# Optimization experiments

Measured on AMD Instinct MI355X. Metric: run time of the kernel, lower is better.

Reference implementation:

```python
import jax, jax.numpy as jnp
import numpy as np

N_NODES = 50000
N_EDGES = 800000
D_FEAT = 64
D_HID = 64
N_CLASSES = 16


def gcn_conv(x, row, col, ew, W, b, n_nodes):
    """PyG GCNConv (normalize=True, add_self_loops=True) with edge weights.
    out[c] = sum_{(r,c) in E+selfloops} d^-1/2[r] * w * d^-1/2[c] * (x @ W)[r] + b
    """
    h = x @ W  # [N, out]
    loop = jnp.arange(n_nodes)
    row = jnp.concatenate([row, loop])
    col = jnp.concatenate([col, loop])
    w = jnp.concatenate([ew, jnp.ones((n_nodes,), dtype=ew.dtype)])
    deg = jax.ops.segment_sum(w, col, num_segments=n_nodes)  # in-degree (weighted)
    dinv = jnp.where(deg > 0, jax.lax.rsqrt(deg), 0.0)
    norm = dinv[row] * w * dinv[col]  # [E+N]
    msgs = norm[:, None] * h[row]  # [E+N, out]
    out = jax.ops.segment_sum(msgs, col, num_segments=n_nodes)
    return out + b


def setup_inputs() -> dict:
    key = jax.random.key(0)
    ks = jax.random.split(key, 12)
    x = jax.random.normal(ks[0], (N_NODES, D_FEAT), dtype=jnp.float32)
    edge_index = jax.random.randint(ks[1], (2, N_EDGES), 0, N_NODES, dtype=jnp.int64)
    edge_attr = jax.random.uniform(ks[2], (N_EDGES,), dtype=jnp.float32)
    s1 = 1.0 / np.sqrt(D_FEAT)
    s2 = 1.0 / np.sqrt(D_HID)
    W1 = jax.random.uniform(ks[3], (D_FEAT, D_HID), minval=-s1, maxval=s1, dtype=jnp.float32)
    b1 = jnp.zeros((D_HID,), dtype=jnp.float32)
    W2 = jax.random.uniform(ks[4], (D_HID, D_HID), minval=-s2, maxval=s2, dtype=jnp.float32)
    b2 = jnp.zeros((D_HID,), dtype=jnp.float32)
    Wm1 = jax.random.uniform(ks[5], (D_HID, D_HID), minval=-s2, maxval=s2, dtype=jnp.float32)
    bm1 = jax.random.uniform(ks[6], (D_HID,), minval=-s2, maxval=s2, dtype=jnp.float32)
    Wm2 = jax.random.uniform(ks[7], (D_HID, N_CLASSES), minval=-s2, maxval=s2, dtype=jnp.float32)
    bm2 = jax.random.uniform(ks[8], (N_CLASSES,), minval=-s2, maxval=s2, dtype=jnp.float32)
    return {"x": x, "edge_index": edge_index, "edge_attr": edge_attr,
            "W1": W1, "b1": b1, "W2": W2, "b2": b2,
            "Wm1": Wm1, "bm1": bm1, "Wm2": Wm2, "bm2": bm2}


def reference(x, edge_index, edge_attr, W1, b1, W2, b2, Wm1, bm1, Wm2, bm2):
    # eval-mode forward: dropout is identity
    n = x.shape[0]
    row, col = edge_index[0], edge_index[1]
    h = jax.nn.relu(gcn_conv(x, row, col, edge_attr, W1, b1, n))
    h = jax.nn.relu(gcn_conv(h, row, col, edge_attr, W2, b2, n))
    h = jax.nn.relu(h @ Wm1 + bm1)
    logits = h @ Wm2 + bm2
    return jax.nn.sigmoid(logits)
```

## Files before the change

kernel.cpp:

```cpp
#include <hip/hip_runtime.h>
#include <hip/hip_fp16.h>
#include <math.h>

#define D 64
#define CAP 48
#define PSZ 512
#define NBIN 98
#define BCAP 9216
#define TSTRIDE 16
#define FILLB 256
#define CHUNKMAX 3136


__global__ void __launch_bounds__(256, 2) k_mm1_fill(
        const float* __restrict__ X, const float* __restrict__ W1,
        __half* __restrict__ Y, int n, int mmBlocks,
        const int* __restrict__ row, const int* __restrict__ col,
        const float* __restrict__ ew, int* __restrict__ tails,
        unsigned long long* __restrict__ binsG, int E) {
    __shared__ unsigned long long buf[CHUNKMAX];
    __shared__ int hist[NBIN], startS[NBIN], curS[NBIN], baseS[NBIN];

    if (blockIdx.x < mmBlocks) {
        int lane = threadIdx.x & 63;
        float wreg[64];
#pragma unroll
        for (int k = 0; k < 64; ++k) wreg[k] = W1[k * 64 + lane];
        int wv  = blockIdx.x * 4 + (threadIdx.x >> 6);
        int nwv = mmBlocks * 4;
        const float4* x4 = (const float4*)X;
        for (int r = wv; r < n; r += nwv) {
            float acc = 0.f;
#pragma unroll
            for (int j = 0; j < 16; ++j) {
                float4 v = x4[r * 16 + j];
                acc += v.x * wreg[4 * j + 0] + v.y * wreg[4 * j + 1]
                     + v.z * wreg[4 * j + 2] + v.w * wreg[4 * j + 3];
            }
            Y[r * 64 + lane] = __float2half(acc);
        }
    } else {
        int fb  = blockIdx.x - mmBlocks;
        int tid = threadIdx.x;
        int chunk = (E + FILLB - 1) / FILLB;
        int e0 = fb * chunk;
        int e1 = min(e0 + chunk, E);
        int tot = e1 - e0;

        for (int i = tid; i < NBIN; i += 256) hist[i] = 0;
        __syncthreads();
        for (int e = e0 + tid; e < e1; e += 256)
            atomicAdd(&hist[col[e] >> 9], 1);
        __syncthreads();
        if (tid < NBIN) {
            int s = 0;
            for (int i = 0; i < tid; ++i) s += hist[i];
            startS[tid] = s;
            curS[tid]   = s;
            baseS[tid]  = atomicAdd(&tails[tid * TSTRIDE], hist[tid]);
        }
        __syncthreads();
        for (int e = e0 + tid; e < e1; e += 256) {
            int c = col[e];
            int b = c >> 9;
            int p = atomicAdd(&curS[b], 1);
            unsigned lo = ((unsigned)row[e] << 9) | (unsigned)(c & (PSZ - 1));
            buf[p] = ((unsigned long long)__float_as_uint(ew[e]) << 32) | lo;
        }
        __syncthreads();
        for (int i = tid; i < tot; i += 256) {
            int loB = 0, hiB = NBIN - 1;
            while (loB < hiB) {
                int mid = (loB + hiB + 1) >> 1;
                if (startS[mid] <= i) loB = mid; else hiB = mid - 1;
            }
            int dst = baseS[loB] + (i - startS[loB]);
            if (dst < BCAP)
                binsG[(size_t)loB * BCAP + dst] = buf[i];
        }
    }
}


__global__ void k_binscatter(const unsigned long long* __restrict__ binsG,
                             const int* __restrict__ tails,
                             int* __restrict__ cnt, int2* __restrict__ bucket, int n) {
    __shared__ int lc[PSZ];
    int bin = blockIdx.x, tid = threadIdx.x;
    for (int i = tid; i < PSZ; i += 256) lc[i] = 0;
    __syncthreads();
    int m = tails[bin * TSTRIDE];
    if (m > BCAP) m = BCAP;
    const unsigned long long* src = binsG + (size_t)bin * BCAP;
    int base = bin * PSZ;
    for (int i = tid; i < m; i += 256) {
        unsigned long long v = src[i];
        unsigned lo = (unsigned)v;
        int cOff = lo & (PSZ - 1);
        int r    = (int)(lo >> 9);
        int p = atomicAdd(&lc[cOff], 1);
        if (p < CAP)
            bucket[(size_t)(base + cOff) * CAP + p] = make_int2(r, (int)(v >> 32));
    }
    __syncthreads();
    for (int i = tid; i < PSZ; i += 256) {
        int node = base + i;
        if (node < n) cnt[node] = lc[i];
    }
}


__global__ void k_dinv_scale(const int* __restrict__ cnt, const int2* __restrict__ bucket,
                             __half* __restrict__ xw1, float* __restrict__ dinv, int n) {
    int lane = threadIdx.x & 63;
    int wv = blockIdx.x * 4 + (threadIdx.x >> 6);
    int nw = gridDim.x * 4;
    for (int node = wv; node < n; node += nw) {
        int c = cnt[node]; if (c > CAP) c = CAP;
        float s = 0.f;
        if (lane < c) s = __int_as_float(bucket[node * CAP + lane].y);
#pragma unroll
        for (int off = 32; off; off >>= 1) s += __shfl_xor(s, off, 64);
        float dv = rsqrtf(1.0f + s);
        if (lane == 0) dinv[node] = dv;
        int idx = node * 64 + lane;
        xw1[idx] = __float2half(dv * __half2float(xw1[idx]));
    }
}


__device__ __forceinline__ float gather_node(const __half* __restrict__ xw,
                                             const int* __restrict__ cnt,
                                             const int2* __restrict__ bucket,
                                             float d, float bb, int node, int lane) {
    float acc0 = __half2float(xw[node * 64 + lane]);
    float acc1 = 0.f, acc2 = 0.f, acc3 = 0.f;
    int p  = node * CAP;
    int c  = cnt[node]; if (c > CAP) c = CAP;
    int pe = p + c;
    for (; p + 8 <= pe; p += 8) {
        int2 e0 = bucket[p + 0];
        int2 e1 = bucket[p + 1];
        int2 e2 = bucket[p + 2];
        int2 e3 = bucket[p + 3];
        int2 e4 = bucket[p + 4];
        int2 e5 = bucket[p + 5];
        int2 e6 = bucket[p + 6];
        int2 e7 = bucket[p + 7];
        float v0 = __half2float(xw[e0.x * 64 + lane]);
        float v1 = __half2float(xw[e1.x * 64 + lane]);
        float v2 = __half2float(xw[e2.x * 64 + lane]);
        float v3 = __half2float(xw[e3.x * 64 + lane]);
        float v4 = __half2float(xw[e4.x * 64 + lane]);
        float v5 = __half2float(xw[e5.x * 64 + lane]);
        float v6 = __half2float(xw[e6.x * 64 + lane]);
        float v7 = __half2float(xw[e7.x * 64 + lane]);
        acc0 += __int_as_float(e0.y) * v0;
        acc1 += __int_as_float(e1.y) * v1;
        acc2 += __int_as_float(e2.y) * v2;
        acc3 += __int_as_float(e3.y) * v3;
        acc0 += __int_as_float(e4.y) * v4;
        acc1 += __int_as_float(e5.y) * v5;
        acc2 += __int_as_float(e6.y) * v6;
        acc3 += __int_as_float(e7.y) * v7;
    }
    for (; p + 4 <= pe; p += 4) {
        int2 e0 = bucket[p + 0];
        int2 e1 = bucket[p + 1];
        int2 e2 = bucket[p + 2];
        int2 e3 = bucket[p + 3];
        acc0 += __int_as_float(e0.y) * __half2float(xw[e0.x * 64 + lane]);
        acc1 += __int_as_float(e1.y) * __half2float(xw[e1.x * 64 + lane]);
        acc2 += __int_as_float(e2.y) * __half2float(xw[e2.x * 64 + lane]);
        acc3 += __int_as_float(e3.y) * __half2float(xw[e3.x * 64 + lane]);
    }
    for (; p < pe; ++p) {
        int2 e = bucket[p];
        acc0 += __int_as_float(e.y) * __half2float(xw[e.x * 64 + lane]);
    }
    return d * ((acc0 + acc1) + (acc2 + acc3)) + bb;
}


__global__ void k_gather_mm(const __half* __restrict__ xw, const float* __restrict__ dinv,
                            const float* __restrict__ b, const int* __restrict__ cnt,
                            const int2* __restrict__ bucket, const float* __restrict__ W,
                            __half* __restrict__ out, int n) {
    __shared__ float ws[64][64];
    __shared__ float hs[4][64];
    int tid = threadIdx.x;
    for (int i = tid; i < 4096; i += 256) ws[i >> 6][i & 63] = W[i];

    int lane = tid & 63, w = tid >> 6;
    float bb = b[lane];
    int ngrp = (n + 3) >> 2;
    for (int g = blockIdx.x; g < ngrp; g += gridDim.x) {
        int node = g * 4 + w;
        float d = (node < n) ? dinv[node] : 0.f;
        __syncthreads();
        if (node < n)
            hs[w][lane] = fmaxf(gather_node(xw, cnt, bucket, d, bb, node, lane), 0.0f);
        __syncthreads();
        if (node < n) {
            float s = 0.f;
#pragma unroll
            for (int k = 0; k < 64; ++k) s += hs[w][k] * ws[k][lane];
            out[node * 64 + lane] = __float2half(d * s);
        }
    }
}


__global__ void k_gather_head(const __half* __restrict__ xw, const float* __restrict__ dinv,
                              const float* __restrict__ b, const int* __restrict__ cnt,
                              const int2* __restrict__ bucket,
                              const float* __restrict__ Wm1, const float* __restrict__ bm1,
                              const float* __restrict__ Wm2, const float* __restrict__ bm2,
                              float* __restrict__ out, int n) {
    __shared__ __half w1h[64][64];
    __shared__ float w2[64][16];
    __shared__ float sb1[64];
    __shared__ float sb2[16];
    __shared__ float h2s[4][64];
    __shared__ float h3s[4][64];
    int tid = threadIdx.x;
    for (int i = tid; i < 4096; i += 256) w1h[i >> 6][i & 63] = __float2half(Wm1[i]);
    for (int i = tid; i < 1024; i += 256) w2[i >> 4][i & 15] = Wm2[i];
    if (tid < 64) sb1[tid] = bm1[tid];
    if (tid < 16) sb2[tid] = bm2[tid];

    int lane = tid & 63, w = tid >> 6;
    float bb = b[lane];
    int ngrp = (n + 3) >> 2;
    for (int g = blockIdx.x; g < ngrp; g += gridDim.x) {
        int node = g * 4 + w;
        float d = (node < n) ? dinv[node] : 0.f;
        __syncthreads();
        if (node < n)
            h2s[w][lane] = fmaxf(gather_node(xw, cnt, bucket, d, bb, node, lane), 0.0f);
        __syncthreads();
        if (node < n) {
            float s = sb1[lane];
#pragma unroll
            for (int k = 0; k < 64; ++k) s += h2s[w][k] * __half2float(w1h[k][lane]);
            h3s[w][lane] = fmaxf(s, 0.0f);
        }
        __syncthreads();
        if (node < n && lane < 16) {
            float s2 = sb2[lane];
#pragma unroll
            for (int k = 0; k < 64; ++k) s2 += h3s[w][k] * w2[k][lane];
            out[node * 16 + lane] = 1.0f / (1.0f + expf(-s2));
        }
    }
}


extern "C" void kernel_launch(void* const* d_in, const int* in_sizes, int n_in,
                              void* d_out, int out_size, void* d_ws, size_t ws_size,
                              hipStream_t stream) {
    const float* x   = (const float*)d_in[0];
    const int*   ei  = (const int*)d_in[1];
    const float* ew  = (const float*)d_in[2];
    const float* W1  = (const float*)d_in[3];
    const float* b1  = (const float*)d_in[4];
    const float* W2  = (const float*)d_in[5];
    const float* b2  = (const float*)d_in[6];
    const float* Wm1 = (const float*)d_in[7];
    const float* bm1 = (const float*)d_in[8];
    const float* Wm2 = (const float*)d_in[9];
    const float* bm2 = (const float*)d_in[10];

    int n = in_sizes[0] / D;
    int E = in_sizes[1] / 2;
    const int* row = ei;
    const int* col = ei + E;

    char* wsb = (char*)d_ws;
    int2*   bucket = (int2*)wsb;
    __half* xw1    = (__half*)(bucket + (size_t)n * CAP);
    unsigned long long* binsG = (unsigned long long*)(xw1 + (size_t)n * D);
    __half* xw2    = (__half*)binsG;
    int*    cnt    = (int*)(binsG + (size_t)NBIN * BCAP);
    float*  dinv   = (float*)(cnt + n);
    int*    tails  = (int*)(dinv + n);
    float*  outp   = (float*)d_out;

    int mmBlocks = 1024;

    hipMemsetAsync(tails, 0, (size_t)NBIN * TSTRIDE * sizeof(int), stream);
    k_mm1_fill<<<mmBlocks + FILLB, 256, 0, stream>>>(x, W1, xw1, n, mmBlocks,
                                                     row, col, ew, tails, binsG, E);
    k_binscatter<<<NBIN, 256, 0, stream>>>(binsG, tails, cnt, bucket, n);
    k_dinv_scale<<<2048, 256, 0, stream>>>(cnt, bucket, xw1, dinv, n);
    k_gather_mm<<<2048, 256, 0, stream>>>(xw1, dinv, b1, cnt, bucket, W2, xw2, n);
    k_gather_head<<<2048, 256, 0, stream>>>(xw2, dinv, b2, cnt, bucket,
                                            Wm1, bm1, Wm2, bm2, outp, n);
}
```

Baseline: 250.6 us.

## Finer binning, fuse degree sum into binscatter, wave-level barriers in gathers

Halves the bin size so twice as many bins and fill blocks are used, and caches edge data in registers so the fill pass reads each edge once. It also uses a two-level prefix sum. The weighted degree sum and rsqrt move into binscatter using shared-memory float atomics, and the scale step becomes a vectorized elementwise kernel. The gather kernels swap block-wide __syncthreads for wave barriers and load bucket entries with nontemporal loads. Float atomic summation order changes rounding slightly, and the CHUNKMAX clamp silently drops edges if E grows beyond the sized capacity.

```diff
diff --git a/kernel.cpp b/kernel.cpp
--- a/kernel.cpp
+++ b/kernel.cpp
@@ -4,12 +4,15 @@
 
 #define D 64
 #define CAP 48
-#define PSZ 512
-#define NBIN 98
-#define BCAP 9216
+#define PSZ 256
+#define NBIN 196
+#define BCAP 4864
 #define TSTRIDE 16
-#define FILLB 256
-#define CHUNKMAX 3136
+#define FILLB 512
+#define CHUNKMAX 1568
+#define ITMAX 7
+
+typedef unsigned long long u64;
 
 
 __global__ void __launch_bounds__(256, 2) k_mm1_fill(
@@ -17,9 +20,10 @@
         __half* __restrict__ Y, int n, int mmBlocks,
         const int* __restrict__ row, const int* __restrict__ col,
         const float* __restrict__ ew, int* __restrict__ tails,
-        unsigned long long* __restrict__ binsG, int E) {
-    __shared__ unsigned long long buf[CHUNKMAX];
+        u64* __restrict__ binsG, int E) {
+    __shared__ u64 buf[CHUNKMAX];
     __shared__ int hist[NBIN], startS[NBIN], curS[NBIN], baseS[NBIN];
+    __shared__ int gsum[16];
 
     if (blockIdx.x < mmBlocks) {
         int lane = threadIdx.x & 63;
@@ -45,27 +49,49 @@
         int chunk = (E + FILLB - 1) / FILLB;
         int e0 = fb * chunk;
         int e1 = min(e0 + chunk, E);
+        if (e1 > e0 + CHUNKMAX) e1 = e0 + CHUNKMAX;
         int tot = e1 - e0;
 
         for (int i = tid; i < NBIN; i += 256) hist[i] = 0;
         __syncthreads();
-        for (int e = e0 + tid; e < e1; e += 256)
-            atomicAdd(&hist[col[e] >> 9], 1);
+
+        unsigned lov[ITMAX], ewv[ITMAX];
+        unsigned char binv[ITMAX];
+#pragma unroll
+        for (int it = 0; it < ITMAX; ++it) {
+            int e = e0 + it * 256 + tid;
+            if (e < e1) {
+                int c = col[e];
+                int b = c >> 8;
+                binv[it] = (unsigned char)b;
+                lov[it]  = ((unsigned)row[e] << 8) | (unsigned)(c & (PSZ - 1));
+                ewv[it]  = __float_as_uint(ew[e]);
+                atomicAdd(&hist[b], 1);
+            }
+        }
+        __syncthreads();
+        if (tid < 13) {
+            int s = 0, hi = min(tid * 16 + 16, NBIN);
+            for (int i = tid * 16; i < hi; ++i) s += hist[i];
+            gsum[tid] = s;
+        }
         __syncthreads();
         if (tid < NBIN) {
-            int s = 0;
-            for (int i = 0; i < tid; ++i) s += hist[i];
+            int s = 0, g = tid >> 4;
+            for (int i = 0; i < g; ++i) s += gsum[i];
+            for (int i = g << 4; i < tid; ++i) s += hist[i];
             startS[tid] = s;
             curS[tid]   = s;
             baseS[tid]  = atomicAdd(&tails[tid * TSTRIDE], hist[tid]);
         }
         __syncthreads();
-        for (int e = e0 + tid; e < e1; e += 256) {
-            int c = col[e];
-            int b = c >> 9;
-            int p = atomicAdd(&curS[b], 1);
-            unsigned lo = ((unsigned)row[e] << 9) | (unsigned)(c & (PSZ - 1));
-            buf[p] = ((unsigned long long)__float_as_uint(ew[e]) << 32) | lo;
+#pragma unroll
+        for (int it = 0; it < ITMAX; ++it) {
+            int e = e0 + it * 256 + tid;
+            if (e < e1) {
+                int p = atomicAdd(&curS[binv[it]], 1);
+                buf[p] = ((u64)ewv[it] << 32) | lov[it];
+            }
         }
         __syncthreads();
         for (int i = tid; i < tot; i += 256) {
@@ -82,52 +108,63 @@
 }
 
 
-__global__ void k_binscatter(const unsigned long long* __restrict__ binsG,
+__global__ void k_binscatter(const u64* __restrict__ binsG,
                              const int* __restrict__ tails,
-                             int* __restrict__ cnt, int2* __restrict__ bucket, int n) {
-    __shared__ int lc[PSZ];
+                             int* __restrict__ cnt, float* __restrict__ dinv,
+                             int2* __restrict__ bucket, int n) {
+    __shared__ int   lc[PSZ];
+    __shared__ float lsum[PSZ];
     int bin = blockIdx.x, tid = threadIdx.x;
-    for (int i = tid; i < PSZ; i += 256) lc[i] = 0;
+    for (int i = tid; i < PSZ; i += blockDim.x) { lc[i] = 0; lsum[i] = 0.f; }
     __syncthreads();
     int m = tails[bin * TSTRIDE];
     if (m > BCAP) m = BCAP;
-    const unsigned long long* src = binsG + (size_t)bin * BCAP;
+    const u64* src = binsG + (size_t)bin * BCAP;
     int base = bin * PSZ;
-    for (int i = tid; i < m; i += 256) {
-        unsigned long long v = src[i];
+    for (int i = tid; i < m; i += blockDim.x) {
+        u64 v = __builtin_nontemporal_load(&src[i]);
         unsigned lo = (unsigned)v;
         int cOff = lo & (PSZ - 1);
-        int r    = (int)(lo >> 9);
+        int r    = (int)(lo >> 8);
+        float w  = __uint_as_float((unsigned)(v >> 32));
         int p = atomicAdd(&lc[cOff], 1);
+        atomicAdd(&lsum[cOff], w);
         if (p < CAP)
             bucket[(size_t)(base + cOff) * CAP + p] = make_int2(r, (int)(v >> 32));
     }
     __syncthreads();
-    for (int i = tid; i < PSZ; i += 256) {
+    for (int i = tid; i < PSZ; i += blockDim.x) {
         int node = base + i;
-        if (node < n) cnt[node] = lc[i];
-    }
-}
-
-
-__global__ void k_dinv_scale(const int* __restrict__ cnt, const int2* __restrict__ bucket,
-                             __half* __restrict__ xw1, float* __restrict__ dinv, int n) {
-    int lane = threadIdx.x & 63;
-    int wv = blockIdx.x * 4 + (threadIdx.x >> 6);
-    int nw = gridDim.x * 4;
-    for (int node = wv; node < n; node += nw) {
-        int c = cnt[node]; if (c > CAP) c = CAP;
-        float s = 0.f;
-        if (lane < c) s = __int_as_float(bucket[node * CAP + lane].y);
-#pragma unroll
-        for (int off = 32; off; off >>= 1) s += __shfl_xor(s, off, 64);
-        float dv = rsqrtf(1.0f + s);
-        if (lane == 0) dinv[node] = dv;
-        int idx = node * 64 + lane;
-        xw1[idx] = __float2half(dv * __half2float(xw1[idx]));
-    }
-}
-
+        if (node < n) {
+            cnt[node]  = lc[i];
+            dinv[node] = rsqrtf(1.0f + lsum[i]);
+        }
+    }
+}
+
+
+__global__ void k_scale(__half* __restrict__ xw1, const float* __restrict__ dinv, int n) {
+    int i = blockIdx.x * 256 + threadIdx.x;
+    int tot = n * 8;
+    if (i >= tot) return;
+    float dv = dinv[i >> 3];
+    float4 raw = *((float4*)(xw1 + (size_t)i * 8));
+    __half2* h = (__half2*)&raw;
+#pragma unroll
+    for (int j = 0; j < 4; ++j) {
+        float lo = __half2float(__low2half(h[j]))  * dv;
+        float hi = __half2float(__high2half(h[j])) * dv;
+        h[j] = __halves2half2(__float2half(lo), __float2half(hi));
+    }
+    *((float4*)(xw1 + (size_t)i * 8)) = raw;
+}
+
+
+__device__ __forceinline__ void ldent(const int2* __restrict__ b, int p, int& r, float& w) {
+    long long v = __builtin_nontemporal_load((const long long*)(b + p));
+    r = (int)v;
+    w = __int_as_float((int)(v >> 32));
+}
 
 __device__ __forceinline__ float gather_node(const __half* __restrict__ xw,
                                              const int* __restrict__ cnt,
@@ -139,44 +176,43 @@
     int c  = cnt[node]; if (c > CAP) c = CAP;
     int pe = p + c;
     for (; p + 8 <= pe; p += 8) {
-        int2 e0 = bucket[p + 0];
-        int2 e1 = bucket[p + 1];
-        int2 e2 = bucket[p + 2];
-        int2 e3 = bucket[p + 3];
-        int2 e4 = bucket[p + 4];
-        int2 e5 = bucket[p + 5];
-        int2 e6 = bucket[p + 6];
-        int2 e7 = bucket[p + 7];
-        float v0 = __half2float(xw[e0.x * 64 + lane]);
-        float v1 = __half2float(xw[e1.x * 64 + lane]);
-        float v2 = __half2float(xw[e2.x * 64 + lane]);
-        float v3 = __half2float(xw[e3.x * 64 + lane]);
-        float v4 = __half2float(xw[e4.x * 64 + lane]);
-        float v5 = __half2float(xw[e5.x * 64 + lane]);
-        float v6 = __half2float(xw[e6.x * 64 + lane]);
-        float v7 = __half2float(xw[e7.x * 64 + lane]);
-        acc0 += __int_as_float(e0.y) * v0;
-        acc1 += __int_as_float(e1.y) * v1;
-        acc2 += __int_as_float(e2.y) * v2;
-        acc3 += __int_as_float(e3.y) * v3;
-        acc0 += __int_as_float(e4.y) * v4;
-        acc1 += __int_as_float(e5.y) * v5;
-        acc2 += __int_as_float(e6.y) * v6;
-        acc3 += __int_as_float(e7.y) * v7;
+        int r0, r1, r2, r3, r4, r5, r6, r7;
+        float w0, w1, w2, w3, w4, w5, w6, w7;
+        ldent(bucket, p + 0, r0, w0);
+        ldent(bucket, p + 1, r1, w1);
+        ldent(bucket, p + 2, r2, w2);
+        ldent(bucket, p + 3, r3, w3);
+        ldent(bucket, p + 4, r4, w4);
+        ldent(bucket, p + 5, r5, w5);
+        ldent(bucket, p + 6, r6, w6);
+        ldent(bucket, p + 7, r7, w7);
+        float v0 = __half2float(xw[r0 * 64 + lane]);
+        float v1 = __half2float(xw[r1 * 64 + lane]);
+        float v2 = __half2float(xw[r2 * 64 + lane]);
+        float v3 = __half2float(xw[r3 * 64 + lane]);
+        float v4 = __half2float(xw[r4 * 64 + lane]);
+        float v5 = __half2float(xw[r5 * 64 + lane]);
+        float v6 = __half2float(xw[r6 * 64 + lane]);
+        float v7 = __half2float(xw[r7 * 64 + lane]);
+        acc0 += w0 * v0;  acc1 += w1 * v1;  acc2 += w2 * v2;  acc3 += w3 * v3;
+        acc0 += w4 * v4;  acc1 += w5 * v5;  acc2 += w6 * v6;  acc3 += w7 * v7;
     }
     for (; p + 4 <= pe; p += 4) {
-        int2 e0 = bucket[p + 0];
-        int2 e1 = bucket[p + 1];
-        int2 e2 = bucket[p + 2];
-        int2 e3 = bucket[p + 3];
-        acc0 += __int_as_float(e0.y) * __half2float(xw[e0.x * 64 + lane]);
-        acc1 += __int_as_float(e1.y) * __half2float(xw[e1.x * 64 + lane]);
-        acc2 += __int_as_float(e2.y) * __half2float(xw[e2.x * 64 + lane]);
-        acc3 += __int_as_float(e3.y) * __half2float(xw[e3.x * 64 + lane]);
+        int r0, r1, r2, r3;
+        float w0, w1, w2, w3;
+        ldent(bucket, p + 0, r0, w0);
+        ldent(bucket, p + 1, r1, w1);
+        ldent(bucket, p + 2, r2, w2);
+        ldent(bucket, p + 3, r3, w3);
+        acc0 += w0 * __half2float(xw[r0 * 64 + lane]);
+        acc1 += w1 * __half2float(xw[r1 * 64 + lane]);
+        acc2 += w2 * __half2float(xw[r2 * 64 + lane]);
+        acc3 += w3 * __half2float(xw[r3 * 64 + lane]);
     }
     for (; p < pe; ++p) {
-        int2 e = bucket[p];
-        acc0 += __int_as_float(e.y) * __half2float(xw[e.x * 64 + lane]);
+        int r0; float w0;
+        ldent(bucket, p, r0, w0);
+        acc0 += w0 * __half2float(xw[r0 * 64 + lane]);
     }
     return d * ((acc0 + acc1) + (acc2 + acc3)) + bb;
 }
@@ -193,20 +229,19 @@
 
     int lane = tid & 63, w = tid >> 6;
     float bb = b[lane];
+    __syncthreads();
     int ngrp = (n + 3) >> 2;
     for (int g = blockIdx.x; g < ngrp; g += gridDim.x) {
         int node = g * 4 + w;
-        float d = (node < n) ? dinv[node] : 0.f;
-        __syncthreads();
-        if (node < n)
-            hs[w][lane] = fmaxf(gather_node(xw, cnt, bucket, d, bb, node, lane), 0.0f);
-        __syncthreads();
-        if (node < n) {
-            float s = 0.f;
-#pragma unroll
-            for (int k = 0; k < 64; ++k) s += hs[w][k] * ws[k][lane];
-            out[node * 64 + lane] = __float2half(d * s);
-        }
+        if (node >= n) continue;
+        float d = dinv[node];
+        hs[w][lane] = fmaxf(gather_node(xw, cnt, bucket, d, bb, node, lane), 0.0f);
+        __builtin_amdgcn_wave_barrier();
+        float s = 0.f;
+#pragma unroll
+        for (int k = 0; k < 64; ++k) s += hs[w][k] * ws[k][lane];
+        __builtin_amdgcn_wave_barrier();
+        out[node * 64 + lane] = __float2half(d * s);
     }
 }
 
@@ -231,27 +266,26 @@
 
     int lane = tid & 63, w = tid >> 6;
     float bb = b[lane];
+    __syncthreads();
     int ngrp = (n + 3) >> 2;
     for (int g = blockIdx.x; g < ngrp; g += gridDim.x) {
         int node = g * 4 + w;
-        float d = (node < n) ? dinv[node] : 0.f;
-        __syncthreads();
-        if (node < n)
-            h2s[w][lane] = fmaxf(gather_node(xw, cnt, bucket, d, bb, node, lane), 0.0f);
-        __syncthreads();
-        if (node < n) {
-            float s = sb1[lane];
-#pragma unroll
-            for (int k = 0; k < 64; ++k) s += h2s[w][k] * __half2float(w1h[k][lane]);
-            h3s[w][lane] = fmaxf(s, 0.0f);
-        }
-        __syncthreads();
-        if (node < n && lane < 16) {
+        if (node >= n) continue;
+        float d = dinv[node];
+        h2s[w][lane] = fmaxf(gather_node(xw, cnt, bucket, d, bb, node, lane), 0.0f);
+        __builtin_amdgcn_wave_barrier();
+        float s = sb1[lane];
+#pragma unroll
+        for (int k = 0; k < 64; ++k) s += h2s[w][k] * __half2float(w1h[k][lane]);
+        h3s[w][lane] = fmaxf(s, 0.0f);
+        __builtin_amdgcn_wave_barrier();
+        if (lane < 16) {
             float s2 = sb2[lane];
 #pragma unroll
             for (int k = 0; k < 64; ++k) s2 += h3s[w][k] * w2[k][lane];
             out[node * 16 + lane] = 1.0f / (1.0f + expf(-s2));
         }
+        __builtin_amdgcn_wave_barrier();
     }
 }
 
@@ -279,7 +313,7 @@
     char* wsb = (char*)d_ws;
     int2*   bucket = (int2*)wsb;
     __half* xw1    = (__half*)(bucket + (size_t)n * CAP);
-    unsigned long long* binsG = (unsigned long long*)(xw1 + (size_t)n * D);
+    u64*    binsG  = (u64*)(xw1 + (size_t)n * D);
     __half* xw2    = (__half*)binsG;
     int*    cnt    = (int*)(binsG + (size_t)NBIN * BCAP);
     float*  dinv   = (float*)(cnt + n);
@@ -291,8 +325,8 @@
     hipMemsetAsync(tails, 0, (size_t)NBIN * TSTRIDE * sizeof(int), stream);
     k_mm1_fill<<<mmBlocks + FILLB, 256, 0, stream>>>(x, W1, xw1, n, mmBlocks,
                                                      row, col, ew, tails, binsG, E);
-    k_binscatter<<<NBIN, 256, 0, stream>>>(binsG, tails, cnt, bucket, n);
-    k_dinv_scale<<<2048, 256, 0, stream>>>(cnt, bucket, xw1, dinv, n);
+    k_binscatter<<<NBIN, 512, 0, stream>>>(binsG, tails, cnt, dinv, bucket, n);
+    k_scale<<<(n * 8 + 255) / 256, 256, 0, stream>>>(xw1, dinv, n);
     k_gather_mm<<<2048, 256, 0, stream>>>(xw1, dinv, b1, cnt, bucket, W2, xw2, n);
     k_gather_head<<<2048, 256, 0, stream>>>(xw2, dinv, b2, cnt, bucket,
                                             Wm1, bm1, Wm2, bm2, outp, n);
```

New measurement: 231.4 us. 7.6% less time.
